# Performance work log

Hardware: AMD Instinct MI355X
Metric: run time of the kernel (lower is better)

## Reference

```python
import jax, jax.numpy as jnp
import numpy as np
import math

B, S, D, H = 2, 2048, 1024, 16
HD = D // H  # 64


def setup_inputs() -> dict:
    key = jax.random.key(0)
    ks = jax.random.split(key, 10)
    s = 1.0 / math.sqrt(D)
    return {
        "q": jax.random.normal(ks[0], (B, S, D), jnp.float32),
        "k": jax.random.normal(ks[1], (B, S, D), jnp.float32),
        "v": jax.random.normal(ks[2], (B, S, D), jnp.float32),
        "attention_mask": jnp.zeros((B, 1, 1, S), jnp.float32),
        "Wq": jax.random.normal(ks[3], (D, D), jnp.float32) * s,
        "bq": jnp.zeros((D,), jnp.float32),
        "Wk": jax.random.normal(ks[4], (D, D), jnp.float32) * s,
        "bk": jnp.zeros((D,), jnp.float32),
        "Wv": jax.random.normal(ks[5], (D, D), jnp.float32) * s,
        "bv": jnp.zeros((D,), jnp.float32),
    }


def reference(q, k, v, attention_mask, Wq, bq, Wk, bk, Wv, bv):
    # QKV projections (torch Linear: x @ W^T + b)
    def split_heads(x):  # [B,S,D] -> [B,H,S,HD]
        return x.reshape(B, S, H, HD).transpose(0, 2, 1, 3)

    ql = split_heads(q @ Wq.T + bq)
    kl = split_heads(k @ Wk.T + bk)
    vl = split_heads(v @ Wv.T + bv)

    scale = 1.0 / math.sqrt(HD)
    scores = jnp.einsum("bhqd,bhkd->bhqk", ql, kl) * scale + attention_mask
    probs = jax.nn.softmax(scores, axis=-1)  # dropout prob = 0.0 -> identity
    ctx = jnp.einsum("bhqk,bhkd->bhqd", probs, vl)
    ctx = ctx.transpose(0, 2, 1, 3).reshape(B, S, D)
    return ctx, scores
```

## Files before the change

kernel.cpp:

```cpp
#include <hip/hip_runtime.h>

typedef __bf16 bf16;
typedef __bf16 bf16x4 __attribute__((ext_vector_type(4)));
typedef __bf16 bf16x8 __attribute__((ext_vector_type(8)));
typedef float f32x4 __attribute__((ext_vector_type(4)));

#define LOG2E 1.4426950408889634f

__global__ __launch_bounds__(256, 2)
void proj_kernel(const float* __restrict__ Xq, const float* __restrict__ Xk,
                 const float* __restrict__ Xv,
                 const float* __restrict__ Wq, const float* __restrict__ Wk,
                 const float* __restrict__ Wv,
                 const float* __restrict__ Bq, const float* __restrict__ Bk,
                 const float* __restrict__ Bv,
                 bf16* __restrict__ Oq, bf16* __restrict__ Ok,
                 bf16* __restrict__ Ov)
{
    const int z = blockIdx.z;
    const float* X  = (z == 0) ? Xq : (z == 1) ? Xk : Xv;
    const float* W  = (z == 0) ? Wq : (z == 1) ? Wk : Wv;
    const float* Bi = (z == 0) ? Bq : (z == 1) ? Bk : Bv;

    const int n0 = blockIdx.x * 128;
    const int m0 = blockIdx.y * 128;

    __shared__ bf16 As[128 * 40];
    __shared__ bf16 Bs[128 * 40];

    const int t = threadIdx.x;
    const int w = t >> 6, l = t & 63, quad = l >> 4, ln = l & 15;
    const int wm = (w & 1) * 64, wn = (w >> 1) * 64;

    const f32x4 zero4 = {0.f, 0.f, 0.f, 0.f};
    f32x4 acc[4][4];
    for (int mi = 0; mi < 4; mi++)
        for (int ni = 0; ni < 4; ni++) acc[mi][ni] = zero4;

    for (int k0 = 0; k0 < 1024; k0 += 32) {
        for (int i = 0; i < 4; i++) {
            int idx = i * 256 + t;
            int row = idx >> 3, c4 = idx & 7;
            float4 a  = *(const float4*)&X[(size_t)(m0 + row) * 1024 + k0 + c4 * 4];
            float4 bb = *(const float4*)&W[(size_t)(n0 + row) * 1024 + k0 + c4 * 4];
            bf16x4 av, bv;
            av[0] = (bf16)a.x;  av[1] = (bf16)a.y;  av[2] = (bf16)a.z;  av[3] = (bf16)a.w;
            bv[0] = (bf16)bb.x; bv[1] = (bf16)bb.y; bv[2] = (bf16)bb.z; bv[3] = (bf16)bb.w;
            *(bf16x4*)&As[row * 40 + c4 * 4] = av;
            *(bf16x4*)&Bs[row * 40 + c4 * 4] = bv;
        }
        __syncthreads();

        bf16x8 af[4], bfv[4];
        for (int mi = 0; mi < 4; mi++)
            af[mi] = *(const bf16x8*)&As[(wm + mi * 16 + ln) * 40 + quad * 8];
        for (int ni = 0; ni < 4; ni++)
            bfv[ni] = *(const bf16x8*)&Bs[(wn + ni * 16 + ln) * 40 + quad * 8];
        for (int mi = 0; mi < 4; mi++)
            for (int ni = 0; ni < 4; ni++)
                acc[mi][ni] = __builtin_amdgcn_mfma_f32_16x16x32_bf16(
                    af[mi], bfv[ni], acc[mi][ni], 0, 0, 0);
        __syncthreads();
    }

    bf16* Onat = (z == 0) ? Oq : Ok;
    for (int ni = 0; ni < 4; ni++) {
        int n = n0 + wn + ni * 16 + ln;
        float bias = Bi[n];
        for (int mi = 0; mi < 4; mi++) {
            int mbase = m0 + wm + mi * 16 + quad * 4;
            if (z < 2) {
                for (int r = 0; r < 4; r++)
                    Onat[(size_t)(mbase + r) * 1024 + n] = (bf16)(acc[mi][ni][r] + bias);
            } else {
                int b = mbase >> 11, s0 = mbase & 2047;
                bf16x4 vv;
                for (int r = 0; r < 4; r++) vv[r] = (bf16)(acc[mi][ni][r] + bias);
                *(bf16x4*)&Ov[(size_t)(b * 1024 + n) * 2048 + s0] = vv;
            }
        }
    }
}

__global__ __launch_bounds__(256, 2)
void attn_kernel(const bf16* __restrict__ Qp, const bf16* __restrict__ Kp,
                 const bf16* __restrict__ Vt, const float* __restrict__ mask,
                 float* __restrict__ ctx, float* __restrict__ scores)
{
    const int lid = blockIdx.x;
    const int wg  = (lid & 7) * 64 + (lid >> 3);
    const int qt = wg & 15, h = (wg >> 4) & 15, b = wg >> 8;

    const int q0 = qt * 128;
    const int t = threadIdx.x, w = t >> 6, l = t & 63, quad = l >> 4, ln = l & 15;

    __shared__ bf16 Qs[128 * 72];
    __shared__ bf16 Ks[64 * 72];
    __shared__ bf16 VTs[64 * 72];
    __shared__ bf16 Ps[128 * 72];

    for (int i = 0; i < 4; i++) {
        int idx = i * 256 + t;
        int row = idx >> 3, d8 = idx & 7;
        *(bf16x8*)&Qs[row * 72 + d8 * 8] =
            *(const bf16x8*)&Qp[(size_t)(b * 2048 + q0 + row) * 1024 + h * 64 + d8 * 8];
    }
    __syncthreads();

    bf16x8 qf[2][2];
#pragma unroll
    for (int mi = 0; mi < 2; mi++)
#pragma unroll
        for (int ks = 0; ks < 2; ks++)
            qf[mi][ks] = *(const bf16x8*)&Qs[(w * 32 + mi * 16 + ln) * 72 + ks * 32 + quad * 8];

    const f32x4 zero4 = {0.f, 0.f, 0.f, 0.f};
    f32x4 Ot[4][2];
#pragma unroll
    for (int ni = 0; ni < 4; ni++)
#pragma unroll
        for (int mi = 0; mi < 2; mi++) Ot[ni][mi] = zero4;
    float mst[2] = {-1e30f, -1e30f};
    float lst[2] = {0.f, 0.f};

    for (int kt = 0; kt < 32; kt++) {
        const int kk0 = kt * 64;
        __syncthreads();
        for (int i = 0; i < 2; i++) {
            int idx = i * 256 + t;
            int row = idx >> 3, d8 = idx & 7;
            *(bf16x8*)&Ks[row * 72 + d8 * 8] =
                *(const bf16x8*)&Kp[(size_t)(b * 2048 + kk0 + row) * 1024 + h * 64 + d8 * 8];
            *(bf16x8*)&VTs[row * 72 + d8 * 8] =
                *(const bf16x8*)&Vt[(size_t)(b * 1024 + h * 64 + row) * 2048 + kk0 + d8 * 8];
        }
        __syncthreads();

        f32x4 st[4][2];
#pragma unroll
        for (int ni = 0; ni < 4; ni++)
#pragma unroll
            for (int mi = 0; mi < 2; mi++) st[ni][mi] = zero4;
#pragma unroll
        for (int ks = 0; ks < 2; ks++) {
            bf16x8 kf[4];
#pragma unroll
            for (int ni = 0; ni < 4; ni++)
                kf[ni] = *(const bf16x8*)&Ks[(ni * 16 + ln) * 72 + ks * 32 + quad * 8];
#pragma unroll
            for (int ni = 0; ni < 4; ni++)
#pragma unroll
                for (int mi = 0; mi < 2; mi++)
                    st[ni][mi] = __builtin_amdgcn_mfma_f32_16x16x32_bf16(
                        kf[ni], qf[mi][ks], st[ni][mi], 0, 0, 0);
        }

        f32x4 mv[4];
#pragma unroll
        for (int ni = 0; ni < 4; ni++)
            mv[ni] = *(const f32x4*)&mask[b * 2048 + kk0 + ni * 16 + quad * 4];

#pragma unroll
        for (int mi = 0; mi < 2; mi++) {
            const size_t srow =
                ((size_t)((b * 16 + h) * 2048 + q0 + w * 32 + mi * 16 + ln)) * 2048 + kk0;
#pragma unroll
            for (int ni = 0; ni < 4; ni++) {
                f32x4 v = st[ni][mi];
#pragma unroll
                for (int r = 0; r < 4; r++) v[r] = v[r] * 0.125f + mv[ni][r];
                st[ni][mi] = v;
                __builtin_nontemporal_store(
                    v, (f32x4*)&scores[srow + ni * 16 + quad * 4]);
            }
        }

#pragma unroll
        for (int mi = 0; mi < 2; mi++) {
            float rm = -1e30f;
#pragma unroll
            for (int ni = 0; ni < 4; ni++)
#pragma unroll
                for (int r = 0; r < 4; r++) rm = fmaxf(rm, st[ni][mi][r]);
            rm = fmaxf(rm, __shfl_xor(rm, 16));
            rm = fmaxf(rm, __shfl_xor(rm, 32));
            const float mnew  = fmaxf(mst[mi], rm);
            const float alpha = exp2f((mst[mi] - mnew) * LOG2E);
            mst[mi] = mnew;

            float rs = 0.f;
#pragma unroll
            for (int ni = 0; ni < 4; ni++) {
                bf16x4 pv;
#pragma unroll
                for (int r = 0; r < 4; r++) {
                    float p = exp2f((st[ni][mi][r] - mnew) * LOG2E);
                    rs += p;
                    pv[r] = (bf16)p;
                }
                *(bf16x4*)&Ps[(w * 32 + mi * 16 + ln) * 72 + ni * 16 + quad * 4] = pv;
            }
            rs += __shfl_xor(rs, 16);
            rs += __shfl_xor(rs, 32);
            lst[mi] = lst[mi] * alpha + rs;

#pragma unroll
            for (int ni = 0; ni < 4; ni++)
#pragma unroll
                for (int r = 0; r < 4; r++) Ot[ni][mi][r] *= alpha;
        }

#pragma unroll
        for (int ks = 0; ks < 2; ks++) {
            bf16x8 vf[4], pf[2];
#pragma unroll
            for (int ni = 0; ni < 4; ni++)
                vf[ni] = *(const bf16x8*)&VTs[(ni * 16 + ln) * 72 + ks * 32 + quad * 8];
#pragma unroll
            for (int mi = 0; mi < 2; mi++)
                pf[mi] = *(const bf16x8*)&Ps[(w * 32 + mi * 16 + ln) * 72 + ks * 32 + quad * 8];
#pragma unroll
            for (int ni = 0; ni < 4; ni++)
#pragma unroll
                for (int mi = 0; mi < 2; mi++)
                    Ot[ni][mi] = __builtin_amdgcn_mfma_f32_16x16x32_bf16(
                        vf[ni], pf[mi], Ot[ni][mi], 0, 0, 0);
        }
    }

#pragma unroll
    for (int mi = 0; mi < 2; mi++) {
        const float rl = 1.0f / lst[mi];
        const int row = b * 2048 + q0 + w * 32 + mi * 16 + ln;
#pragma unroll
        for (int ni = 0; ni < 4; ni++) {
            f32x4 o = Ot[ni][mi];
#pragma unroll
            for (int r = 0; r < 4; r++) o[r] *= rl;
            *(f32x4*)&ctx[(size_t)row * 1024 + h * 64 + ni * 16 + quad * 4] = o;
        }
    }
}

extern "C" void kernel_launch(void* const* d_in, const int* in_sizes, int n_in,
                              void* d_out, int out_size, void* d_ws, size_t ws_size,
                              hipStream_t stream) {
    const float* q    = (const float*)d_in[0];
    const float* k    = (const float*)d_in[1];
    const float* v    = (const float*)d_in[2];
    const float* mask = (const float*)d_in[3];
    const float* Wq   = (const float*)d_in[4];
    const float* bq   = (const float*)d_in[5];
    const float* Wk   = (const float*)d_in[6];
    const float* bk   = (const float*)d_in[7];
    const float* Wv   = (const float*)d_in[8];
    const float* bv   = (const float*)d_in[9];

    bf16* Qp = (bf16*)d_ws;
    bf16* Kp = Qp + (size_t)4096 * 1024;
    bf16* Vt = Kp + (size_t)4096 * 1024;

    float* ctx    = (float*)d_out;
    float* scores = ctx + (size_t)2 * 2048 * 1024;

    proj_kernel<<<dim3(8, 32, 3), 256, 0, stream>>>(
        q, k, v, Wq, Wk, Wv, bq, bk, bv, Qp, Kp, Vt);
    attn_kernel<<<dim3(512, 1, 1), 256, 0, stream>>>(
        Qp, Kp, Vt, mask, ctx, scores);
}
```

Measured before the change: 737.6 us.

## Halve attention query tile, double-buffer K in LDS, read V directly

The attention kernel now handles 64 query rows per workgroup instead of 128 and launches twice as many workgroups, raising the occupancy hint to 4. K tiles are double-buffered in shared memory, with the next tile prefetched into registers during compute, so only one barrier is needed per iteration. Q fragments and V fragments are read straight from global memory instead of being staged through LDS. The aim is more parallelism and less barrier stall, at the cost of more global traffic for V and less reuse of each K/V tile across query rows.

Result: no change. 745.0 us (+1.0%).

```diff
diff --git a/kernel.cpp b/kernel.cpp
--- a/kernel.cpp
+++ b/kernel.cpp
@@ -82,77 +82,72 @@
     }
 }
 
-__global__ __launch_bounds__(256, 2)
+__global__ __launch_bounds__(256, 4)
 void attn_kernel(const bf16* __restrict__ Qp, const bf16* __restrict__ Kp,
                  const bf16* __restrict__ Vt, const float* __restrict__ mask,
                  float* __restrict__ ctx, float* __restrict__ scores)
 {
     const int lid = blockIdx.x;
-    const int wg  = (lid & 7) * 64 + (lid >> 3);
-    const int qt = wg & 15, h = (wg >> 4) & 15, b = wg >> 8;
-
-    const int q0 = qt * 128;
+    const int wg  = (lid & 7) * 128 + (lid >> 3);
+    const int qt = wg & 31, h = (wg >> 5) & 15, b = wg >> 9;
+
+    const int q0 = qt * 64;
     const int t = threadIdx.x, w = t >> 6, l = t & 63, quad = l >> 4, ln = l & 15;
 
-    __shared__ bf16 Qs[128 * 72];
-    __shared__ bf16 Ks[64 * 72];
-    __shared__ bf16 VTs[64 * 72];
-    __shared__ bf16 Ps[128 * 72];
-
-    for (int i = 0; i < 4; i++) {
-        int idx = i * 256 + t;
-        int row = idx >> 3, d8 = idx & 7;
-        *(bf16x8*)&Qs[row * 72 + d8 * 8] =
-            *(const bf16x8*)&Qp[(size_t)(b * 2048 + q0 + row) * 1024 + h * 64 + d8 * 8];
+    __shared__ bf16 Ks[2][64 * 72];
+    __shared__ bf16 Ps[64 * 72];
+
+    const int qrow = q0 + w * 16 + ln;
+
+    bf16x8 qf[2];
+#pragma unroll
+    for (int ks = 0; ks < 2; ks++)
+        qf[ks] = *(const bf16x8*)&Qp[(size_t)(b * 2048 + qrow) * 1024 + h * 64 + ks * 32 + quad * 8];
+
+    const int krow = t >> 2, kseg = t & 3;
+    const bf16* kbase = &Kp[(size_t)(b * 2048 + krow) * 1024 + h * 64 + kseg * 16];
+
+    {
+        bf16x8 r0 = *(const bf16x8*)&kbase[0];
+        bf16x8 r1 = *(const bf16x8*)&kbase[8];
+        *(bf16x8*)&Ks[0][krow * 72 + kseg * 16 + 0] = r0;
+        *(bf16x8*)&Ks[0][krow * 72 + kseg * 16 + 8] = r1;
     }
     __syncthreads();
 
-    bf16x8 qf[2][2];
-#pragma unroll
-    for (int mi = 0; mi < 2; mi++)
-#pragma unroll
-        for (int ks = 0; ks < 2; ks++)
-            qf[mi][ks] = *(const bf16x8*)&Qs[(w * 32 + mi * 16 + ln) * 72 + ks * 32 + quad * 8];
-
     const f32x4 zero4 = {0.f, 0.f, 0.f, 0.f};
-    f32x4 Ot[4][2];
-#pragma unroll
-    for (int ni = 0; ni < 4; ni++)
-#pragma unroll
-        for (int mi = 0; mi < 2; mi++) Ot[ni][mi] = zero4;
-    float mst[2] = {-1e30f, -1e30f};
-    float lst[2] = {0.f, 0.f};
+    f32x4 Ot[4];
+#pragma unroll
+    for (int ni = 0; ni < 4; ni++) Ot[ni] = zero4;
+    float mst = -1e30f, lst = 0.f;
+
+    const size_t srow = ((size_t)((b * 16 + h) * 2048 + qrow)) * 2048;
+    const bf16* vbase = &Vt[(size_t)(b * 1024 + h * 64) * 2048];
 
     for (int kt = 0; kt < 32; kt++) {
         const int kk0 = kt * 64;
-        __syncthreads();
-        for (int i = 0; i < 2; i++) {
-            int idx = i * 256 + t;
-            int row = idx >> 3, d8 = idx & 7;
-            *(bf16x8*)&Ks[row * 72 + d8 * 8] =
-                *(const bf16x8*)&Kp[(size_t)(b * 2048 + kk0 + row) * 1024 + h * 64 + d8 * 8];
-            *(bf16x8*)&VTs[row * 72 + d8 * 8] =
-                *(const bf16x8*)&Vt[(size_t)(b * 1024 + h * 64 + row) * 2048 + kk0 + d8 * 8];
-        }
-        __syncthreads();
-
-        f32x4 st[4][2];
-#pragma unroll
-        for (int ni = 0; ni < 4; ni++)
-#pragma unroll
-            for (int mi = 0; mi < 2; mi++) st[ni][mi] = zero4;
+        const int cur = kt & 1;
+
+        bf16x8 pr0, pr1;
+        if (kt < 31) {
+            const bf16* src = kbase + (size_t)(kk0 + 64) * 1024;
+            pr0 = *(const bf16x8*)&src[0];
+            pr1 = *(const bf16x8*)&src[8];
+        }
+
+        f32x4 st[4];
+#pragma unroll
+        for (int ni = 0; ni < 4; ni++) st[ni] = zero4;
 #pragma unroll
         for (int ks = 0; ks < 2; ks++) {
             bf16x8 kf[4];
 #pragma unroll
             for (int ni = 0; ni < 4; ni++)
-                kf[ni] = *(const bf16x8*)&Ks[(ni * 16 + ln) * 72 + ks * 32 + quad * 8];
-#pragma unroll
-            for (int ni = 0; ni < 4; ni++)
-#pragma unroll
-                for (int mi = 0; mi < 2; mi++)
-                    st[ni][mi] = __builtin_amdgcn_mfma_f32_16x16x32_bf16(
-                        kf[ni], qf[mi][ks], st[ni][mi], 0, 0, 0);
+                kf[ni] = *(const bf16x8*)&Ks[cur][(ni * 16 + ln) * 72 + ks * 32 + quad * 8];
+#pragma unroll
+            for (int ni = 0; ni < 4; ni++)
+                st[ni] = __builtin_amdgcn_mfma_f32_16x16x32_bf16(
+                    kf[ni], qf[ks], st[ni], 0, 0, 0);
         }
 
         f32x4 mv[4];
@@ -161,84 +156,73 @@
             mv[ni] = *(const f32x4*)&mask[b * 2048 + kk0 + ni * 16 + quad * 4];
 
 #pragma unroll
-        for (int mi = 0; mi < 2; mi++) {
-            const size_t srow =
-                ((size_t)((b * 16 + h) * 2048 + q0 + w * 32 + mi * 16 + ln)) * 2048 + kk0;
-#pragma unroll
-            for (int ni = 0; ni < 4; ni++) {
-                f32x4 v = st[ni][mi];
-#pragma unroll
-                for (int r = 0; r < 4; r++) v[r] = v[r] * 0.125f + mv[ni][r];
-                st[ni][mi] = v;
-                __builtin_nontemporal_store(
-                    v, (f32x4*)&scores[srow + ni * 16 + quad * 4]);
+        for (int ni = 0; ni < 4; ni++) {
+            f32x4 v = st[ni];
+#pragma unroll
+            for (int r = 0; r < 4; r++) v[r] = v[r] * 0.125f + mv[ni][r];
+            st[ni] = v;
+            __builtin_nontemporal_store(v, (f32x4*)&scores[srow + kk0 + ni * 16 + quad * 4]);
+        }
+
+        float rm = -1e30f;
+#pragma unroll
+        for (int ni = 0; ni < 4; ni++)
+#pragma unroll
+            for (int r = 0; r < 4; r++) rm = fmaxf(rm, st[ni][r]);
+        rm = fmaxf(rm, __shfl_xor(rm, 16));
+        rm = fmaxf(rm, __shfl_xor(rm, 32));
+        const float mnew  = fmaxf(mst, rm);
+        const float alpha = exp2f((mst - mnew) * LOG2E);
+        mst = mnew;
+
+        float rs = 0.f;
+#pragma unroll
+        for (int ni = 0; ni < 4; ni++) {
+            bf16x4 pv;
+#pragma unroll
+            for (int r = 0; r < 4; r++) {
+                float p = exp2f((st[ni][r] - mnew) * LOG2E);
+                rs += p;
+                pv[r] = (bf16)p;
             }
-        }
-
-#pragma unroll
-        for (int mi = 0; mi < 2; mi++) {
-            float rm = -1e30f;
-#pragma unroll
-            for (int ni = 0; ni < 4; ni++)
-#pragma unroll
-                for (int r = 0; r < 4; r++) rm = fmaxf(rm, st[ni][mi][r]);
-            rm = fmaxf(rm, __shfl_xor(rm, 16));
-            rm = fmaxf(rm, __shfl_xor(rm, 32));
-            const float mnew  = fmaxf(mst[mi], rm);
-            const float alpha = exp2f((mst[mi] - mnew) * LOG2E);
-            mst[mi] = mnew;
-
-            float rs = 0.f;
-#pragma unroll
-            for (int ni = 0; ni < 4; ni++) {
-                bf16x4 pv;
-#pragma unroll
-                for (int r = 0; r < 4; r++) {
-                    float p = exp2f((st[ni][mi][r] - mnew) * LOG2E);
-                    rs += p;
-                    pv[r] = (bf16)p;
-                }
-                *(bf16x4*)&Ps[(w * 32 + mi * 16 + ln) * 72 + ni * 16 + quad * 4] = pv;
-            }
-            rs += __shfl_xor(rs, 16);
-            rs += __shfl_xor(rs, 32);
-            lst[mi] = lst[mi] * alpha + rs;
-
-#pragma unroll
-            for (int ni = 0; ni < 4; ni++)
-#pragma unroll
-                for (int r = 0; r < 4; r++) Ot[ni][mi][r] *= alpha;
-        }
+            *(bf16x4*)&Ps[(w * 16 + ln) * 72 + ni * 16 + quad * 4] = pv;
+        }
+        rs += __shfl_xor(rs, 16);
+        rs += __shfl_xor(rs, 32);
+        lst = lst * alpha + rs;
+
+#pragma unroll
+        for (int ni = 0; ni < 4; ni++)
+#pragma unroll
+            for (int r = 0; r < 4; r++) Ot[ni][r] *= alpha;
 
 #pragma unroll
         for (int ks = 0; ks < 2; ks++) {
-            bf16x8 vf[4], pf[2];
-#pragma unroll
-            for (int ni = 0; ni < 4; ni++)
-                vf[ni] = *(const bf16x8*)&VTs[(ni * 16 + ln) * 72 + ks * 32 + quad * 8];
-#pragma unroll
-            for (int mi = 0; mi < 2; mi++)
-                pf[mi] = *(const bf16x8*)&Ps[(w * 32 + mi * 16 + ln) * 72 + ks * 32 + quad * 8];
-#pragma unroll
-            for (int ni = 0; ni < 4; ni++)
-#pragma unroll
-                for (int mi = 0; mi < 2; mi++)
-                    Ot[ni][mi] = __builtin_amdgcn_mfma_f32_16x16x32_bf16(
-                        vf[ni], pf[mi], Ot[ni][mi], 0, 0, 0);
-        }
-    }
-
-#pragma unroll
-    for (int mi = 0; mi < 2; mi++) {
-        const float rl = 1.0f / lst[mi];
-        const int row = b * 2048 + q0 + w * 32 + mi * 16 + ln;
-#pragma unroll
-        for (int ni = 0; ni < 4; ni++) {
-            f32x4 o = Ot[ni][mi];
-#pragma unroll
-            for (int r = 0; r < 4; r++) o[r] *= rl;
-            *(f32x4*)&ctx[(size_t)row * 1024 + h * 64 + ni * 16 + quad * 4] = o;
-        }
+            bf16x8 vf[4];
+#pragma unroll
+            for (int ni = 0; ni < 4; ni++)
+                vf[ni] = *(const bf16x8*)&vbase[(size_t)(ni * 16 + ln) * 2048 + kk0 + ks * 32 + quad * 8];
+            bf16x8 pf = *(const bf16x8*)&Ps[(w * 16 + ln) * 72 + ks * 32 + quad * 8];
+#pragma unroll
+            for (int ni = 0; ni < 4; ni++)
+                Ot[ni] = __builtin_amdgcn_mfma_f32_16x16x32_bf16(
+                    vf[ni], pf, Ot[ni], 0, 0, 0);
+        }
+
+        if (kt < 31) {
+            *(bf16x8*)&Ks[cur ^ 1][krow * 72 + kseg * 16 + 0] = pr0;
+            *(bf16x8*)&Ks[cur ^ 1][krow * 72 + kseg * 16 + 8] = pr1;
+            __syncthreads();
+        }
+    }
+
+    const float rl = 1.0f / lst;
+#pragma unroll
+    for (int ni = 0; ni < 4; ni++) {
+        f32x4 o = Ot[ni];
+#pragma unroll
+        for (int r = 0; r < 4; r++) o[r] *= rl;
+        *(f32x4*)&ctx[(size_t)(b * 2048 + qrow) * 1024 + h * 64 + ni * 16 + quad * 4] = o;
     }
 }
 
@@ -265,6 +249,6 @@
 
     proj_kernel<<<dim3(8, 32, 3), 256, 0, stream>>>(
         q, k, v, Wq, Wk, Wv, bq, bk, bv, Qp, Kp, Vt);
-    attn_kernel<<<dim3(512, 1, 1), 256, 0, stream>>>(
+    attn_kernel<<<dim3(1024, 1, 1), 256, 0, stream>>>(
         Qp, Kp, Vt, mask, ctx, scores);
 }
```

## Pre-convert projection inputs to bf16 and stream tiles via global_load_lds

Applied to the files above, without the earlier changes.

Adds a conversion kernel that casts the q/k/v activations and the three weight matrices to bf16 once. The projection GEMM then copies operand tiles straight from global memory into LDS with global_load_lds, stored in an MFMA-fragment-ordered layout, instead of loading fp32 into registers and converting per tile. This halves the bytes the GEMM reads and removes per-tile conversion and register staging. The cost is an extra launch and a full read/write pass over the inputs. The bf16 copies live in the tail of the scores output buffer, relying on attn_kernel overwriting that region afterward.

Measured after the change: 737.0 us. No clear change (-0.1%).

```diff
diff --git a/kernel.cpp b/kernel.cpp
--- a/kernel.cpp
+++ b/kernel.cpp
@@ -7,62 +7,97 @@
 
 #define LOG2E 1.4426950408889634f
 
+#define GLOAD_LDS(gptr, lptr)                                                   \
+    __builtin_amdgcn_global_load_lds(                                           \
+        (const __attribute__((address_space(1))) void*)(gptr),                  \
+        (__attribute__((address_space(3))) void*)(lptr), 16, 0, 0)
+
+__global__ __launch_bounds__(256)
+void cvt_kernel(const float* __restrict__ q, const float* __restrict__ k,
+                const float* __restrict__ v, const float* __restrict__ wq,
+                const float* __restrict__ wk, const float* __restrict__ wv,
+                bf16* __restrict__ xq, bf16* __restrict__ xk,
+                bf16* __restrict__ xv, bf16* __restrict__ wqb,
+                bf16* __restrict__ wkb, bf16* __restrict__ wvb)
+{
+    const int z = blockIdx.y;
+    if (z >= 3 && blockIdx.x >= 256) return;
+    const float* src = (z == 0) ? q : (z == 1) ? k : (z == 2) ? v
+                     : (z == 3) ? wq : (z == 4) ? wk : wv;
+    bf16* dst = (z == 0) ? xq : (z == 1) ? xk : (z == 2) ? xv
+              : (z == 3) ? wqb : (z == 4) ? wkb : wvb;
+    const size_t base = (size_t)blockIdx.x * 4096 + threadIdx.x * 4;
+#pragma unroll
+    for (int p = 0; p < 4; p++) {
+        float4 a = *(const float4*)&src[base + p * 1024];
+        bf16x4 o;
+        o[0] = (bf16)a.x; o[1] = (bf16)a.y; o[2] = (bf16)a.z; o[3] = (bf16)a.w;
+        *(bf16x4*)&dst[base + p * 1024] = o;
+    }
+}
+
 __global__ __launch_bounds__(256, 2)
-void proj_kernel(const float* __restrict__ Xq, const float* __restrict__ Xk,
-                 const float* __restrict__ Xv,
-                 const float* __restrict__ Wq, const float* __restrict__ Wk,
-                 const float* __restrict__ Wv,
+void proj_kernel(const bf16* __restrict__ Xq, const bf16* __restrict__ Xk,
+                 const bf16* __restrict__ Xv,
+                 const bf16* __restrict__ Wq, const bf16* __restrict__ Wk,
+                 const bf16* __restrict__ Wv,
                  const float* __restrict__ Bq, const float* __restrict__ Bk,
                  const float* __restrict__ Bv,
                  bf16* __restrict__ Oq, bf16* __restrict__ Ok,
                  bf16* __restrict__ Ov)
 {
     const int z = blockIdx.z;
-    const float* X  = (z == 0) ? Xq : (z == 1) ? Xk : Xv;
-    const float* W  = (z == 0) ? Wq : (z == 1) ? Wk : Wv;
+    const bf16* X  = (z == 0) ? Xq : (z == 1) ? Xk : Xv;
+    const bf16* W  = (z == 0) ? Wq : (z == 1) ? Wk : Wv;
     const float* Bi = (z == 0) ? Bq : (z == 1) ? Bk : Bv;
 
     const int n0 = blockIdx.x * 128;
     const int m0 = blockIdx.y * 128;
 
-    __shared__ bf16 As[128 * 40];
-    __shared__ bf16 Bs[128 * 40];
+    __shared__ bf16 As[8 * 512];
+    __shared__ bf16 Bs[8 * 512];
 
     const int t = threadIdx.x;
     const int w = t >> 6, l = t & 63, quad = l >> 4, ln = l & 15;
-    const int wm = (w & 1) * 64, wn = (w >> 1) * 64;
+
+    const int fa0 = w * 2, fa1 = w * 2 + 1;
+    const bf16* gA0 = &X[(size_t)(m0 + fa0 * 16 + ln) * 1024 + quad * 8];
+    const bf16* gA1 = &X[(size_t)(m0 + fa1 * 16 + ln) * 1024 + quad * 8];
+    const bf16* gB0 = &W[(size_t)(n0 + fa0 * 16 + ln) * 1024 + quad * 8];
+    const bf16* gB1 = &W[(size_t)(n0 + fa1 * 16 + ln) * 1024 + quad * 8];
 
     const f32x4 zero4 = {0.f, 0.f, 0.f, 0.f};
     f32x4 acc[4][4];
     for (int mi = 0; mi < 4; mi++)
         for (int ni = 0; ni < 4; ni++) acc[mi][ni] = zero4;
 
+    const int wafr = (w & 1) * 4;
+    const int wbfr = (w >> 1) * 4;
+
     for (int k0 = 0; k0 < 1024; k0 += 32) {
-        for (int i = 0; i < 4; i++) {
-            int idx = i * 256 + t;
-            int row = idx >> 3, c4 = idx & 7;
-            float4 a  = *(const float4*)&X[(size_t)(m0 + row) * 1024 + k0 + c4 * 4];
-            float4 bb = *(const float4*)&W[(size_t)(n0 + row) * 1024 + k0 + c4 * 4];
-            bf16x4 av, bv;
-            av[0] = (bf16)a.x;  av[1] = (bf16)a.y;  av[2] = (bf16)a.z;  av[3] = (bf16)a.w;
-            bv[0] = (bf16)bb.x; bv[1] = (bf16)bb.y; bv[2] = (bf16)bb.z; bv[3] = (bf16)bb.w;
-            *(bf16x4*)&As[row * 40 + c4 * 4] = av;
-            *(bf16x4*)&Bs[row * 40 + c4 * 4] = bv;
-        }
+        GLOAD_LDS(gA0 + k0, &As[fa0 * 512]);
+        GLOAD_LDS(gA1 + k0, &As[fa1 * 512]);
+        GLOAD_LDS(gB0 + k0, &Bs[fa0 * 512]);
+        GLOAD_LDS(gB1 + k0, &Bs[fa1 * 512]);
         __syncthreads();
 
         bf16x8 af[4], bfv[4];
+#pragma unroll
         for (int mi = 0; mi < 4; mi++)
-            af[mi] = *(const bf16x8*)&As[(wm + mi * 16 + ln) * 40 + quad * 8];
+            af[mi] = *(const bf16x8*)&As[(wafr + mi) * 512 + l * 8];
+#pragma unroll
         for (int ni = 0; ni < 4; ni++)
-            bfv[ni] = *(const bf16x8*)&Bs[(wn + ni * 16 + ln) * 40 + quad * 8];
+            bfv[ni] = *(const bf16x8*)&Bs[(wbfr + ni) * 512 + l * 8];
+#pragma unroll
         for (int mi = 0; mi < 4; mi++)
+#pragma unroll
             for (int ni = 0; ni < 4; ni++)
                 acc[mi][ni] = __builtin_amdgcn_mfma_f32_16x16x32_bf16(
                     af[mi], bfv[ni], acc[mi][ni], 0, 0, 0);
         __syncthreads();
     }
 
+    const int wm = (w & 1) * 64, wn = (w >> 1) * 64;
     bf16* Onat = (z == 0) ? Oq : Ok;
     for (int ni = 0; ni < 4; ni++) {
         int n = n0 + wn + ni * 16 + ln;
@@ -256,15 +291,24 @@
     const float* Wv   = (const float*)d_in[8];
     const float* bv   = (const float*)d_in[9];
 
-    bf16* Qp = (bf16*)d_ws;
-    bf16* Kp = Qp + (size_t)4096 * 1024;
-    bf16* Vt = Kp + (size_t)4096 * 1024;
+    bf16* Qp  = (bf16*)d_ws;
+    bf16* Kp  = Qp  + (size_t)4096 * 1024;
+    bf16* Vt  = Kp  + (size_t)4096 * 1024;
 
     float* ctx    = (float*)d_out;
     float* scores = ctx + (size_t)2 * 2048 * 1024;
 
+    bf16* Xbq = (bf16*)(scores + 126353408);
+    bf16* Xbk = Xbq + (size_t)4096 * 1024;
+    bf16* Xbv = Xbk + (size_t)4096 * 1024;
+    bf16* Wbq = Xbv + (size_t)4096 * 1024;
+    bf16* Wbk = Wbq + (size_t)1024 * 1024;
+    bf16* Wbv = Wbk + (size_t)1024 * 1024;
+
+    cvt_kernel<<<dim3(1024, 6), 256, 0, stream>>>(
+        q, k, v, Wq, Wk, Wv, Xbq, Xbk, Xbv, Wbq, Wbk, Wbv);
     proj_kernel<<<dim3(8, 32, 3), 256, 0, stream>>>(
-        q, k, v, Wq, Wk, Wv, bq, bk, bv, Qp, Kp, Vt);
+        Xbq, Xbk, Xbv, Wbq, Wbk, Wbv, bq, bk, bv, Qp, Kp, Vt);
     attn_kernel<<<dim3(512, 1, 1), 256, 0, stream>>>(
         Qp, Kp, Vt, mask, ctx, scores);
 }
```
